# Optimization experiments

Measured on AMD Instinct MI355X. Metric: run time of the kernel, lower is better.

Reference implementation:

```python
import jax, jax.numpy as jnp
import numpy as np

UNITS = 512
M = 8
INPUT_DIM = 512
BATCH = 2048


def setup_inputs() -> dict:
    key = jax.random.key(0)
    ks = jax.random.split(key, 9)
    D, U = INPUT_DIM, UNITS
    fused_dim = D + U
    def glorot(k, shape):
        lim = np.sqrt(6.0 / (shape[0] + shape[1])).astype(np.float32)
        return jax.random.uniform(k, shape, jnp.float32, -lim, lim)
    return {
        "inputs": jax.random.normal(ks[0], (BATCH, D), jnp.float32),
        "elapsed": jax.random.uniform(ks[1], (BATCH, 1), jnp.float32),
        "state": jax.random.normal(ks[2], (BATCH, U * M), jnp.float32),
        "W_r": glorot(ks[3], (fused_dim, U * M)),
        "b_r": jnp.zeros((U * M,), jnp.float32),
        "W_d": glorot(ks[4], (fused_dim, U)),
        "b_d": jnp.zeros((U,), jnp.float32),
        "W_u": glorot(ks[5], (fused_dim, U * M)),
        "b_u": jnp.zeros((U * M,), jnp.float32),
    }


def reference(inputs, elapsed, state, W_r, b_r, W_d, b_d, W_u, b_u):
    B = inputs.shape[0]
    # tau_i = 10**(i/2)  =>  ln_tau_i = i * 0.5 * ln(10)
    ln_tau_table = 0.5 * jnp.log(jnp.float32(10.0)) * jnp.arange(M, dtype=jnp.float32)  # [M]
    tau_table = jnp.exp(ln_tau_table)  # [M]

    h_hat = state.reshape(B, UNITS, M)            # [B, U, M]
    h = h_hat.sum(axis=2)                          # [B, U]
    fused = jnp.concatenate([inputs, h], axis=-1)  # [B, D+U]

    # retrieval gate: softmax over M buckets of -(ln_tau_r - table)^2
    ln_tau_r = (fused @ W_r + b_r).reshape(B, UNITS, M)
    rki = jax.nn.softmax(-jnp.square(ln_tau_r - ln_tau_table), axis=2)
    q_input = jnp.sum(rki * h_hat, axis=2)         # [B, U]

    # detect (candidate) with tanh
    reset_value = jnp.concatenate([inputs, q_input], axis=1)
    qk = jnp.tanh(reset_value @ W_d + b_d)[:, :, None]  # [B, U, 1]

    # update gate
    ln_tau_s = (fused @ W_u + b_u).reshape(B, UNITS, M)
    ski = jax.nn.softmax(-jnp.square(ln_tau_s - ln_tau_table), axis=2)

    # exponential decay per bucket: elapsed [B,1] / tau [M] -> [B, M]
    exp_term = jnp.exp(-elapsed / tau_table)[:, None, :]  # [B, 1, M]
    h_hat_next = ((1.0 - ski) * h_hat + ski * qk) * exp_term  # [B, U, M]

    h_next = h_hat_next.sum(axis=2)                # [B, U]
    return h_next, h_hat_next.reshape(B, UNITS * M)
```

## Files before the change

kernel.cpp:

```cpp
#include <hip/hip_runtime.h>
#include <hip/hip_fp16.h>
#include <cmath>

#define B_SZ 2048
#define D_IN 512
#define U_N  512
#define FD   1024
#define NRU  4096
#define NRU2 8192

typedef _Float16 f16x8 __attribute__((ext_vector_type(8)));
typedef float    f32x4 __attribute__((ext_vector_type(4)));

typedef const __attribute__((address_space(1))) void glb_cv;
typedef __attribute__((address_space(3))) void lds_v;

#define TAB_INIT {0.0f, 1.15129254649702f, 2.30258509299405f, \
                  3.45387763949107f, 4.60517018598809f, 5.75646273248511f, \
                  6.90775527898214f, 8.05904782547916f}

__global__ __launch_bounds__(256) void prep_kernel(
    const float* __restrict__ inputs, const float* __restrict__ state,
    __half* __restrict__ fused, __half* __restrict__ reset)
{
    const int b = blockIdx.x;
    const int t = threadIdx.x;

    const float2 iv = *(const float2*)(inputs + (size_t)b * D_IN + t * 2);
    __half2 hv;
    hv.x = __float2half(iv.x);
    hv.y = __float2half(iv.y);
    *(__half2*)(fused + (size_t)b * FD + t * 2) = hv;
    *(__half2*)(reset + (size_t)b * FD + t * 2) = hv;

    const float4* sp = (const float4*)(state + (size_t)b * NRU + t * 16);
    float4 x0 = sp[0], x1 = sp[1], x2 = sp[2], x3 = sp[3];
    float s0 = (x0.x + x0.y) + (x0.z + x0.w) + (x1.x + x1.y) + (x1.z + x1.w);
    float s1 = (x2.x + x2.y) + (x2.z + x2.w) + (x3.x + x3.y) + (x3.z + x3.w);
    __half2 h2;
    h2.x = __float2half(s0);
    h2.y = __float2half(s1);
    *(__half2*)(fused + (size_t)b * FD + D_IN + t * 2) = h2;
}

__global__ __launch_bounds__(256) void convT3_kernel(
    const float* __restrict__ W_r, const float* __restrict__ W_u,
    const float* __restrict__ W_d, __half* __restrict__ WruT,
    __half* __restrict__ WdT)
{
    __shared__ float tile[32][33];
    const int bx = blockIdx.x;
    const float* W;
    __half* Wt;
    int N, nt;
    if (bx < 128)      { W = W_r; Wt = WruT;                    N = NRU; nt = bx * 32; }
    else if (bx < 256) { W = W_u; Wt = WruT + (size_t)NRU * FD; N = NRU; nt = (bx - 128) * 32; }
    else               { W = W_d; Wt = WdT;                     N = U_N; nt = (bx - 256) * 32; }

    const int kt = blockIdx.y * 32;
    const int t  = threadIdx.x;
    const int c  = t & 31;
    const int r4 = t >> 5;

#pragma unroll
    for (int i = 0; i < 4; i++) {
        int r = r4 + i * 8;
        tile[r][c] = W[(size_t)(kt + r) * N + nt + c];
    }
    __syncthreads();
#pragma unroll
    for (int i = 0; i < 4; i++) {
        int rr = r4 + i * 8;
        Wt[(size_t)(nt + rr) * FD + kt + c] = __float2half(tile[c][rr]);
    }
}

template <int BM, int EPI>
__global__ __launch_bounds__(256) void gemm_k(
    const __half* __restrict__ A, const __half* __restrict__ Bt,
    const float* __restrict__ biasA, const float* __restrict__ biasB, int nsplit,
    float* __restrict__ C, int Ncols,
    const float* __restrict__ state, __half* __restrict__ resetw,
    __half* __restrict__ skibuf, int K)
{
    extern __shared__ __align__(16) char smem[];
    __half* sA = (__half*)smem;
    __half* sB = (__half*)(smem + BM * 128);

    const int t    = threadIdx.x;
    const int m0   = blockIdx.y * BM;
    const int n0   = blockIdx.x << 7;
    const int lane = t & 63;
    const int w    = t >> 6;
    const int m16  = lane & 15;
    const int quad = lane >> 4;
    constexpr int MI = BM / 32;
    constexpr int IA = BM / 32;
    const int wm = (w & 1) * (BM / 2);
    const int wn = (w >> 1) << 6;
    const int strip = w >> 1;

    f32x4 acc[MI][4];
#pragma unroll
    for (int i = 0; i < MI; i++)
#pragma unroll
        for (int j = 0; j < 4; j++)
#pragma unroll
            for (int r = 0; r < 4; r++) acc[i][j][r] = 0.f;

    const __half* gAp[IA];
    const __half* lAp[IA];
#pragma unroll
    for (int i = 0; i < IA; i++) {
        const int off = w * (BM * 32) + i * 1024 + lane * 16;
        const int row = off >> 7;
        const int g   = ((off & 127) >> 4) ^ (row & 7);
        gAp[i] = A + (size_t)(m0 + row) * K + g * 8;
        lAp[i] = sA + ((w * (BM * 32) + i * 1024) >> 1);
    }
    const __half* gBp[4];
    const __half* lBp[4];
#pragma unroll
    for (int i = 0; i < 4; i++) {
        const int off = w * 4096 + i * 1024 + lane * 16;
        const int row = off >> 7;
        const int g   = ((off & 127) >> 4) ^ (row & 7);
        gBp[i] = Bt + (size_t)(n0 + row) * K + g * 8;
        lBp[i] = sB + ((w * 4096 + i * 1024) >> 1);
    }

    for (int kt = 0; kt < K; kt += 64) {
        __syncthreads();
#pragma unroll
        for (int i = 0; i < IA; i++)
            __builtin_amdgcn_global_load_lds((glb_cv*)(gAp[i] + kt), (lds_v*)lAp[i], 16, 0, 0);
#pragma unroll
        for (int i = 0; i < 4; i++)
            __builtin_amdgcn_global_load_lds((glb_cv*)(gBp[i] + kt), (lds_v*)lBp[i], 16, 0, 0);
        __syncthreads();

#pragma unroll
        for (int s = 0; s < 2; s++) {
            f16x8 af[MI], bf[4];
#pragma unroll
            for (int mi = 0; mi < MI; mi++) {
                const int row = wm + mi * 16 + m16;
                const int gi  = (s * 4 + quad) ^ (row & 7);
                af[mi] = *(const f16x8*)(sA + row * 64 + gi * 8);
            }
#pragma unroll
            for (int ni = 0; ni < 4; ni++) {
                const int row = wn + ni * 16 + m16;
                const int gi  = (s * 4 + quad) ^ (row & 7);
                bf[ni] = *(const f16x8*)(sB + row * 64 + gi * 8);
            }
#pragma unroll
            for (int mi = 0; mi < MI; mi++)
#pragma unroll
                for (int ni = 0; ni < 4; ni++)
                    acc[mi][ni] = __builtin_amdgcn_mfma_f32_16x16x32_f16(
                        af[mi], bf[ni], acc[mi][ni], 0, 0, 0);
        }
    }

    if constexpr (EPI == 0) {
#pragma unroll
        for (int mi = 0; mi < MI; mi++) {
#pragma unroll
            for (int ni = 0; ni < 4; ni++) {
                const int col = n0 + wn + ni * 16 + m16;
                const float bv = biasA[col];
#pragma unroll
                for (int r = 0; r < 4; r++) {
                    const int row = m0 + wm + mi * 16 + quad * 4 + r;
                    C[(size_t)row * Ncols + col] = tanhf(acc[mi][ni][r] + bv);
                }
            }
        }
    } else {
        __syncthreads();
        float*  ebuf = (float*)smem;
        __half* qbuf = (__half*)(smem + 128 * 36 * 4);
        const bool is_r = (n0 < nsplit);
        const float* bp = is_r ? biasA : biasB;
        const int n0r = is_r ? n0 : n0 - nsplit;
        const float TAB[8] = TAB_INIT;
        const int ug  = t & 3;
        const int s   = ug >> 1;
        const int g   = ug & 1;
        const int bl0 = t >> 2;

        for (int ni = 0; ni < 4; ni++) {
            const float bv = bp[n0r + strip * 64 + ni * 16 + m16];
#pragma unroll
            for (int mi = 0; mi < 4; mi++)
#pragma unroll
                for (int r = 0; r < 4; r++)
                    ebuf[(wm + mi * 16 + quad * 4 + r) * 36 + strip * 16 + m16] =
                        acc[mi][ni][r] + bv;
            __syncthreads();

#pragma unroll
            for (int p = 0; p < 2; p++) {
                const int b_loc = bl0 + p * 64;
                const int b = m0 + b_loc;
                const float* rowp = ebuf + b_loc * 36 + ug * 8;
                float v[8];
                *(float4*)&v[0] = *(const float4*)rowp;
                *(float4*)&v[4] = *(const float4*)(rowp + 4);

                float e[8];
                float sum = 0.f;
#pragma unroll
                for (int i = 0; i < 8; i++) {
                    float d = v[i] - TAB[i];
                    e[i] = __expf(-d * d);
                    sum += e[i];
                }
                const int col = n0r + s * 64 + ni * 16 + g * 8;
                if (is_r) {
                    const float4 h0 = *(const float4*)(state + (size_t)b * NRU + col);
                    const float4 h1 = *(const float4*)(state + (size_t)b * NRU + col + 4);
                    const float hv[8] = {h0.x, h0.y, h0.z, h0.w, h1.x, h1.y, h1.z, h1.w};
                    float qn = 0.f;
#pragma unroll
                    for (int i = 0; i < 8; i++) qn += e[i] * hv[i];
                    qbuf[b_loc * 16 + (s * 8 + ni * 2 + g)] = __float2half(qn / sum);
                } else {
                    const float inv = 1.0f / sum;
                    __half2 o[4];
#pragma unroll
                    for (int i = 0; i < 4; i++) {
                        o[i].x = __float2half(e[2 * i] * inv);
                        o[i].y = __float2half(e[2 * i + 1] * inv);
                    }
                    *(uint4*)(skibuf + (size_t)b * NRU + col) = *(uint4*)o;
                }
            }
            __syncthreads();
        }
        if (is_r) {
            const int b_loc = t >> 1;
            const int j = t & 1;
            uint4 qv = *(uint4*)(qbuf + b_loc * 16 + j * 8);
            *(uint4*)(resetw + (size_t)(m0 + b_loc) * FD + D_IN + (n0r >> 3) + j * 8) = qv;
        }
    }
}

__global__ __launch_bounds__(256) void final_kernel(
    const __half* __restrict__ skibuf, const float* __restrict__ state,
    const float* __restrict__ qk, const float* __restrict__ elapsed,
    float* __restrict__ out0, float* __restrict__ out1)
{
    const int idx = blockIdx.x * 256 + threadIdx.x;
    const int b = idx >> 9;
    const int u = idx & 511;

    const float INV_TAU[8] = {1.0f, 0.316227766016838f, 0.1f, 0.0316227766016838f,
                              0.01f, 0.00316227766016838f, 0.001f, 0.000316227766016838f};

    const uint4 sr = *(const uint4*)(skibuf + (size_t)b * NRU + u * 8);
    const __half2* sh = (const __half2*)&sr;
    float sk[8];
#pragma unroll
    for (int i = 0; i < 4; i++) {
        float2 f2 = __half22float2(sh[i]);
        sk[2 * i]     = f2.x;
        sk[2 * i + 1] = f2.y;
    }

    const float4* hh = (const float4*)(state + ((size_t)b * NRU + u * 8));
    float4 h0 = hh[0], h1 = hh[1];
    float h[8] = {h0.x, h0.y, h0.z, h0.w, h1.x, h1.y, h1.z, h1.w};

    const float q  = qk[(size_t)b * U_N + u];
    const float el = elapsed[b];

    float hn[8];
    float acc = 0.f;
#pragma unroll
    for (int i = 0; i < 8; i++) {
        const float et = __expf(-el * INV_TAU[i]);
        hn[i] = ((1.0f - sk[i]) * h[i] + sk[i] * q) * et;
        acc += hn[i];
    }

    float4* o = (float4*)(out1 + ((size_t)b * NRU + u * 8));
    o[0] = make_float4(hn[0], hn[1], hn[2], hn[3]);
    o[1] = make_float4(hn[4], hn[5], hn[6], hn[7]);
    out0[(size_t)b * U_N + u] = acc;
}

extern "C" void kernel_launch(void* const* d_in, const int* in_sizes, int n_in,
                              void* d_out, int out_size, void* d_ws, size_t ws_size,
                              hipStream_t stream)
{
    (void)in_sizes; (void)n_in; (void)out_size; (void)ws_size;

    const float* inputs  = (const float*)d_in[0];
    const float* elapsed = (const float*)d_in[1];
    const float* state   = (const float*)d_in[2];
    const float* W_r     = (const float*)d_in[3];
    const float* b_r     = (const float*)d_in[4];
    const float* W_d     = (const float*)d_in[5];
    const float* b_d     = (const float*)d_in[6];
    const float* W_u     = (const float*)d_in[7];
    const float* b_u     = (const float*)d_in[8];
    float* out = (float*)d_out;

    char* ws = (char*)d_ws;
    __half* fused  = (__half*)(ws);
    __half* reset  = (__half*)(ws + ((size_t)4  << 20));
    __half* WruT   = (__half*)(ws + ((size_t)8  << 20));
    __half* WdT    = (__half*)(ws + ((size_t)24 << 20));
    __half* skibuf = (__half*)(ws + ((size_t)25 << 20));
    float*  qk     = (float*) (ws + ((size_t)41 << 20));

    prep_kernel<<<B_SZ, 256, 0, stream>>>(inputs, state, fused, reset);
    convT3_kernel<<<dim3(272, FD / 32), 256, 0, stream>>>(W_r, W_u, W_d, WruT, WdT);

    gemm_k<128, 1><<<dim3(NRU2 / 128, B_SZ / 128), 256, 32768, stream>>>(
        fused, WruT, b_r, b_u, NRU, nullptr, 0, state, reset, skibuf, FD);

    gemm_k<64, 0><<<dim3(U_N / 128, B_SZ / 64), 256, 24576, stream>>>(
        reset, WdT, b_d, nullptr, 1 << 30, qk, U_N, nullptr, nullptr, nullptr, FD);

    final_kernel<<<(B_SZ * U_N) / 256, 256, 0, stream>>>(skibuf, state, qk, elapsed, out,
                                                         out + (size_t)B_SZ * U_N);
}
```

Measured before the change: 211.8 us.

## Replace fused gate GEMM with 256x256 tiled, pipelined LDS-direct kernel

The main fused-input GEMM for both gates is replaced by a new 512-thread kernel with 256x256 output tiles. It double-buffers operands in 128KB of LDS, loading them directly from global memory into LDS, and interleaves those loads with MFMA quarters using explicit barriers, waitcnts and wave priority. The softmax/retrieval epilogue is carried over to the new tile shape. The goal is more data reuse per tile and overlap of memory with compute. The cost is heavy LDS use, which limits occupancy, and fewer blocks (256) to spread across the CUs.

```diff
diff --git a/kernel.cpp b/kernel.cpp
--- a/kernel.cpp
+++ b/kernel.cpp
@@ -72,6 +72,186 @@
     for (int i = 0; i < 4; i++) {
         int rr = r4 + i * 8;
         Wt[(size_t)(nt + rr) * FD + kt + c] = __float2half(tile[c][rr]);
+    }
+}
+
+__global__ __launch_bounds__(512, 2) void gemm_big(
+    const __half* __restrict__ A, const __half* __restrict__ Bt,
+    const float* __restrict__ b_r, const float* __restrict__ b_u,
+    const float* __restrict__ state, __half* __restrict__ resetw,
+    __half* __restrict__ skibuf)
+{
+    __shared__ __align__(16) char smem[131072];
+    __half* SAh = (__half*)smem;
+
+    const int t    = threadIdx.x;
+    const int m0   = blockIdx.y << 8;
+    const int n0   = blockIdx.x << 8;
+    const int lane = t & 63;
+    const int w    = t >> 6;
+    const int wm16 = ((w >> 2) & 1) << 4;
+    const int wn16 = (w & 3) << 4;
+    const int m16  = lane & 15;
+    const int quad = lane >> 4;
+    const int g0   = (quad ^ (m16 & 7)) << 3;
+    const int g1   = ((quad + 4) ^ (m16 & 7)) << 3;
+    const int t8   = t << 3;
+    const int trow = t >> 3;
+    const int gcol = ((t & 7) ^ (trow & 7)) << 3;
+
+    const __half* gA = A  + (size_t)(m0 + trow) * FD + gcol;
+    const __half* gB = Bt + (size_t)(n0 + trow) * FD + gcol;
+
+    f32x4 acc[8][4];
+#pragma unroll
+    for (int a1 = 0; a1 < 8; a1++)
+#pragma unroll
+        for (int a2 = 0; a2 < 4; a2++)
+            acc[a1][a2] = (f32x4){0.f, 0.f, 0.f, 0.f};
+
+#define BARRIER() __builtin_amdgcn_s_barrier()
+#define PRIO1 __builtin_amdgcn_s_setprio(1)
+#define PRIO0 __builtin_amdgcn_s_setprio(0)
+#define WAITV(n) do { asm volatile("s_waitcnt vmcnt(" #n ")" ::: "memory"); \
+                      __builtin_amdgcn_sched_barrier(0); } while (0)
+#define WAITL() do { asm volatile("s_waitcnt lgkmcnt(0)" ::: "memory"); \
+                     __builtin_amdgcn_sched_barrier(0); } while (0)
+
+#define STAGE_A(buf, h, tt) do { \
+        const __half* _s = gA + (size_t)((h) * 128) * FD + (tt) * 64; \
+        __half* _d = SAh + (buf) * 32768 + (h) * 8192 + t8; \
+        __builtin_amdgcn_global_load_lds((glb_cv*)_s, (lds_v*)_d, 16, 0, 0); \
+        __builtin_amdgcn_global_load_lds((glb_cv*)(_s + (size_t)64 * FD), \
+                                         (lds_v*)(_d + 4096), 16, 0, 0); } while (0)
+#define STAGE_B(buf, h, tt) do { \
+        const __half* _s = gB + (size_t)((h) * 128) * FD + (tt) * 64; \
+        __half* _d = SAh + (buf) * 32768 + 16384 + (h) * 8192 + t8; \
+        __builtin_amdgcn_global_load_lds((glb_cv*)_s, (lds_v*)_d, 16, 0, 0); \
+        __builtin_amdgcn_global_load_lds((glb_cv*)(_s + (size_t)64 * FD), \
+                                         (lds_v*)(_d + 4096), 16, 0, 0); } while (0)
+
+#define READ_A(c, mh) do { _Pragma("unroll") \
+    for (int mi2 = 0; mi2 < 4; mi2++) { \
+        const __half* _ap = SAh + (c) * 32768 + \
+            ((((mh) * 4 + mi2) * 32 + wm16 + m16) << 6); \
+        af[mi2][0] = *(const f16x8*)(_ap + g0); \
+        af[mi2][1] = *(const f16x8*)(_ap + g1); } } while (0)
+#define READ_B(c, nh) do { _Pragma("unroll") \
+    for (int ni2 = 0; ni2 < 2; ni2++) { \
+        const __half* _bp = SAh + (c) * 32768 + 16384 + \
+            ((((nh) * 2 + ni2) * 64 + wn16 + m16) << 6); \
+        bf[ni2][0] = *(const f16x8*)(_bp + g0); \
+        bf[ni2][1] = *(const f16x8*)(_bp + g1); } } while (0)
+
+#define MFMAQ(MH, NH) do { _Pragma("unroll") \
+    for (int mi2 = 0; mi2 < 4; mi2++) { _Pragma("unroll") \
+        for (int ni2 = 0; ni2 < 2; ni2++) { \
+            acc[(MH)*4+mi2][(NH)*2+ni2] = __builtin_amdgcn_mfma_f32_16x16x32_f16( \
+                af[mi2][0], bf[ni2][0], acc[(MH)*4+mi2][(NH)*2+ni2], 0, 0, 0); \
+            acc[(MH)*4+mi2][(NH)*2+ni2] = __builtin_amdgcn_mfma_f32_16x16x32_f16( \
+                af[mi2][1], bf[ni2][1], acc[(MH)*4+mi2][(NH)*2+ni2], 0, 0, 0); } } } while (0)
+
+    STAGE_A(0, 0, 0); STAGE_B(0, 0, 0); STAGE_A(0, 1, 0); STAGE_B(0, 1, 0);
+    STAGE_A(1, 0, 1); STAGE_B(1, 1, 1); STAGE_A(1, 1, 1);
+    WAITV(6);
+    BARRIER();
+
+#pragma unroll 1
+    for (int i = 0; i < 8; i++) {
+        const int ta = (2 * i + 1) & 15, tb = (2 * i + 2) & 15, tc = (2 * i + 3) & 15;
+        f16x8 af[4][2], bf[2][2];
+        READ_A(0, 0); READ_B(0, 0); STAGE_B(1, 0, ta);
+        BARRIER(); WAITL(); PRIO1; MFMAQ(0, 0); PRIO0; BARRIER();
+        READ_B(0, 1); STAGE_A(0, 0, tb);
+        BARRIER(); WAITL(); PRIO1; MFMAQ(0, 1); PRIO0; BARRIER();
+        READ_A(0, 1); STAGE_B(0, 1, tb);
+        BARRIER(); WAITL(); PRIO1; MFMAQ(1, 1); PRIO0; BARRIER();
+        READ_B(0, 0); STAGE_A(0, 1, tb);
+        BARRIER(); WAITL(); PRIO1; MFMAQ(1, 0); PRIO0; WAITV(6); BARRIER();
+        READ_A(1, 0); READ_B(1, 0); STAGE_B(0, 0, tb);
+        BARRIER(); WAITL(); PRIO1; MFMAQ(0, 0); PRIO0; BARRIER();
+        READ_B(1, 1); STAGE_A(1, 0, tc);
+        BARRIER(); WAITL(); PRIO1; MFMAQ(0, 1); PRIO0; BARRIER();
+        READ_A(1, 1); STAGE_B(1, 1, tc);
+        BARRIER(); WAITL(); PRIO1; MFMAQ(1, 1); PRIO0; BARRIER();
+        READ_B(1, 0); STAGE_A(1, 1, tc);
+        BARRIER(); WAITL(); PRIO1; MFMAQ(1, 0); PRIO0; WAITV(6); BARRIER();
+    }
+
+    WAITV(0);
+    __syncthreads();
+
+#undef BARRIER
+#undef PRIO1
+#undef PRIO0
+#undef WAITV
+#undef WAITL
+#undef STAGE_A
+#undef STAGE_B
+#undef READ_A
+#undef READ_B
+#undef MFMAQ
+
+    float*  ebuf = (float*)smem;
+    __half* qbuf = (__half*)(smem + 256 * 68 * 4);
+    const bool is_r = (n0 < NRU);
+    const float* bp = is_r ? b_r : b_u;
+    const int n0r = is_r ? n0 : n0 - NRU;
+    const float TAB[8] = TAB_INIT;
+
+    for (int ni = 0; ni < 4; ni++) {
+        const float bv = bp[n0r + ni * 64 + wn16 + m16];
+#pragma unroll
+        for (int mi = 0; mi < 8; mi++)
+#pragma unroll
+            for (int r = 0; r < 4; r++)
+                ebuf[(mi * 32 + wm16 + quad * 4 + r) * 68 + wn16 + m16] =
+                    acc[mi][ni][r] + bv;
+        __syncthreads();
+
+#pragma unroll
+        for (int p = 0; p < 4; p++) {
+            const int item = p * 512 + t;
+            const int row = item >> 3, g = item & 7;
+            const int b = m0 + row;
+            const float* rp = ebuf + row * 68 + g * 8;
+            float v[8];
+            *(float4*)&v[0] = *(const float4*)rp;
+            *(float4*)&v[4] = *(const float4*)(rp + 4);
+
+            float e[8], sum = 0.f;
+#pragma unroll
+            for (int i2 = 0; i2 < 8; i2++) {
+                float d = v[i2] - TAB[i2];
+                e[i2] = __expf(-d * d);
+                sum += e[i2];
+            }
+            const int colr = n0r + ni * 64 + g * 8;
+            if (is_r) {
+                const float4 h0 = *(const float4*)(state + (size_t)b * NRU + colr);
+                const float4 h1 = *(const float4*)(state + (size_t)b * NRU + colr + 4);
+                const float hv[8] = {h0.x, h0.y, h0.z, h0.w, h1.x, h1.y, h1.z, h1.w};
+                float qn = 0.f;
+#pragma unroll
+                for (int i2 = 0; i2 < 8; i2++) qn += e[i2] * hv[i2];
+                qbuf[row * 8 + g] = __float2half(qn / sum);
+            } else {
+                const float inv = 1.0f / sum;
+                __half2 o[4];
+#pragma unroll
+                for (int i2 = 0; i2 < 4; i2++) {
+                    o[i2].x = __float2half(e[2 * i2] * inv);
+                    o[i2].y = __float2half(e[2 * i2 + 1] * inv);
+                }
+                *(uint4*)(skibuf + (size_t)b * NRU + colr) = *(uint4*)o;
+            }
+        }
+        __syncthreads();
+        if (is_r) {
+            const int row = t >> 1, lg = (t & 1) << 2;
+            uint2 qv = *(uint2*)(qbuf + row * 8 + lg);
+            *(uint2*)(resetw + (size_t)(m0 + row) * FD + D_IN + (n0r >> 3) + ni * 8 + lg) = qv;
+        }
     }
 }
 
@@ -98,7 +278,6 @@
     constexpr int IA = BM / 32;
     const int wm = (w & 1) * (BM / 2);
     const int wn = (w >> 1) << 6;
-    const int strip = w >> 1;
 
     f32x4 acc[MI][4];
 #pragma unroll
@@ -176,74 +355,6 @@
                     C[(size_t)row * Ncols + col] = tanhf(acc[mi][ni][r] + bv);
                 }
             }
-        }
-    } else {
-        __syncthreads();
-        float*  ebuf = (float*)smem;
-        __half* qbuf = (__half*)(smem + 128 * 36 * 4);
-        const bool is_r = (n0 < nsplit);
-        const float* bp = is_r ? biasA : biasB;
-        const int n0r = is_r ? n0 : n0 - nsplit;
-        const float TAB[8] = TAB_INIT;
-        const int ug  = t & 3;
-        const int s   = ug >> 1;
-        const int g   = ug & 1;
-        const int bl0 = t >> 2;
-
-        for (int ni = 0; ni < 4; ni++) {
-            const float bv = bp[n0r + strip * 64 + ni * 16 + m16];
-#pragma unroll
-            for (int mi = 0; mi < 4; mi++)
-#pragma unroll
-                for (int r = 0; r < 4; r++)
-                    ebuf[(wm + mi * 16 + quad * 4 + r) * 36 + strip * 16 + m16] =
-                        acc[mi][ni][r] + bv;
-            __syncthreads();
-
-#pragma unroll
-            for (int p = 0; p < 2; p++) {
-                const int b_loc = bl0 + p * 64;
-                const int b = m0 + b_loc;
-                const float* rowp = ebuf + b_loc * 36 + ug * 8;
-                float v[8];
-                *(float4*)&v[0] = *(const float4*)rowp;
-                *(float4*)&v[4] = *(const float4*)(rowp + 4);
-
-                float e[8];
-                float sum = 0.f;
-#pragma unroll
-                for (int i = 0; i < 8; i++) {
-                    float d = v[i] - TAB[i];
-                    e[i] = __expf(-d * d);
-                    sum += e[i];
-                }
-                const int col = n0r + s * 64 + ni * 16 + g * 8;
-                if (is_r) {
-                    const float4 h0 = *(const float4*)(state + (size_t)b * NRU + col);
-                    const float4 h1 = *(const float4*)(state + (size_t)b * NRU + col + 4);
-                    const float hv[8] = {h0.x, h0.y, h0.z, h0.w, h1.x, h1.y, h1.z, h1.w};
-                    float qn = 0.f;
-#pragma unroll
-                    for (int i = 0; i < 8; i++) qn += e[i] * hv[i];
-                    qbuf[b_loc * 16 + (s * 8 + ni * 2 + g)] = __float2half(qn / sum);
-                } else {
-                    const float inv = 1.0f / sum;
-                    __half2 o[4];
-#pragma unroll
-                    for (int i = 0; i < 4; i++) {
-                        o[i].x = __float2half(e[2 * i] * inv);
-                        o[i].y = __float2half(e[2 * i + 1] * inv);
-                    }
-                    *(uint4*)(skibuf + (size_t)b * NRU + col) = *(uint4*)o;
-                }
-            }
-            __syncthreads();
-        }
-        if (is_r) {
-            const int b_loc = t >> 1;
-            const int j = t & 1;
-            uint4 qv = *(uint4*)(qbuf + b_loc * 16 + j * 8);
-            *(uint4*)(resetw + (size_t)(m0 + b_loc) * FD + D_IN + (n0r >> 3) + j * 8) = qv;
         }
     }
 }
@@ -320,8 +431,8 @@
     prep_kernel<<<B_SZ, 256, 0, stream>>>(inputs, state, fused, reset);
     convT3_kernel<<<dim3(272, FD / 32), 256, 0, stream>>>(W_r, W_u, W_d, WruT, WdT);
 
-    gemm_k<128, 1><<<dim3(NRU2 / 128, B_SZ / 128), 256, 32768, stream>>>(
-        fused, WruT, b_r, b_u, NRU, nullptr, 0, state, reset, skibuf, FD);
+    gemm_big<<<dim3(NRU2 / 256, B_SZ / 256), 512, 0, stream>>>(
+        fused, WruT, b_r, b_u, state, reset, skibuf);
 
     gemm_k<64, 0><<<dim3(U_N / 128, B_SZ / 64), 256, 24576, stream>>>(
         reset, WdT, b_d, nullptr, 1 << 30, qk, U_N, nullptr, nullptr, nullptr, FD);
```

Result: faster. 200.3 us (-5.4%).
